# Optimization experiments

Hardware: AMD Instinct MI355X
Metric: run time of the kernel (lower is better)

The kernel has to match this reference:

```python
import jax, jax.numpy as jnp
import numpy as np

N = 50000          # nodes
E = 800000         # edges (avg degree 16)
IN_NODE = 64
IN_EDGE = 16
HID = 64
HEADS = 2
NEG_SLOPE = 0.2
EPS = 1e-16


def setup_inputs() -> dict:
    key = jax.random.key(0)
    ks = jax.random.split(key, 32)
    i = iter(range(32))
    rn = lambda shape, s=1.0: jax.random.normal(ks[next(i)], shape, jnp.float32) * s
    inp = {
        "h": rn((N, IN_NODE)),
        "e": rn((E, IN_EDGE)),
        "edge_index": jax.random.randint(ks[next(i)], (2, E), 0, N),
        "w": rn((E, IN_EDGE)),
        # initial GATConv: in_node -> hidden, heads=2 (averaged)
        "W0": rn((IN_NODE, HEADS * HID), 0.05),
        "att_src0": rn((HEADS, HID), 0.05),
        "att_dst0": rn((HEADS, HID), 0.05),
        "We0": rn((IN_EDGE, HEADS * HID), 0.05),
        "att_e0": rn((HEADS, HID), 0.05),
        "b0": jnp.zeros((HID,), jnp.float32),
        # hidden GATConv 1: hidden -> hidden, heads=1
        "W1": rn((HID, HID), 0.05),
        "att_src1": rn((1, HID), 0.05),
        "att_dst1": rn((1, HID), 0.05),
        "We1": rn((IN_EDGE, HID), 0.05),
        "att_e1": rn((1, HID), 0.05),
        "b1": jnp.zeros((HID,), jnp.float32),
        # hidden GATConv 2
        "W2": rn((HID, HID), 0.05),
        "att_src2": rn((1, HID), 0.05),
        "att_dst2": rn((1, HID), 0.05),
        "We2": rn((IN_EDGE, HID), 0.05),
        "att_e2": rn((1, HID), 0.05),
        "b2": jnp.zeros((HID,), jnp.float32),
        # readout Linear(hidden, in_node)
        "Wr": rn((HID, IN_NODE), 0.05),
        "br": jnp.zeros((IN_NODE,), jnp.float32),
    }
    return inp


def gat_conv(x, edge_attr, src, dst, W, a_src, a_dst, We, a_e, b, concat):
    """PyG-style GATConv with edge features (no self-loops)."""
    H, C = a_src.shape
    xw = (x @ W).reshape(-1, H, C)                      # [N, H, C]
    ew = (edge_attr @ We).reshape(-1, H, C)             # [E, H, C]
    alpha_n_src = jnp.einsum('nhc,hc->nh', xw, a_src)   # [N, H]
    alpha_n_dst = jnp.einsum('nhc,hc->nh', xw, a_dst)   # [N, H]
    alpha_e = jnp.einsum('ehc,hc->eh', ew, a_e)         # [E, H]
    alpha = alpha_n_src[src] + alpha_n_dst[dst] + alpha_e
    alpha = jax.nn.leaky_relu(alpha, NEG_SLOPE)         # [E, H]
    # segment softmax over incoming edges of each dst node
    m = jax.ops.segment_max(alpha, dst, num_segments=N)
    ex = jnp.exp(alpha - m[dst])
    den = jax.ops.segment_sum(ex, dst, num_segments=N)
    coef = ex / (den[dst] + EPS)                        # [E, H]
    msg = coef[:, :, None] * xw[src]                    # [E, H, C]
    out = jax.ops.segment_sum(msg, dst, num_segments=N) # [N, H, C]
    out = out.reshape(N, H * C) if concat else out.mean(axis=1)
    return out + b


def reference(h, e, edge_index, w,
              W0, att_src0, att_dst0, We0, att_e0, b0,
              W1, att_src1, att_dst1, We1, att_e1, b1,
              W2, att_src2, att_dst2, We2, att_e2, b2,
              Wr, br):
    src, dst = edge_index[0], edge_index[1]
    x = jax.nn.silu(gat_conv(h, w, src, dst, W0, att_src0, att_dst0, We0, att_e0, b0, concat=False))
    x = jax.nn.silu(gat_conv(x, w, src, dst, W1, att_src1, att_dst1, We1, att_e1, b1, concat=False))
    x = jax.nn.silu(gat_conv(x, w, src, dst, W2, att_src2, att_dst2, We2, att_e2, b2, concat=False))
    x = x @ Wr + br                                     # readout [N, IN_NODE]
    return (x, e)
```

## Files before the change

### kernel.cpp

```cpp
#include <hip/hip_runtime.h>
#include <hip/hip_bf16.h>

#define IN_NODE 64
#define IN_EDGE 16
#define HID 64
#define BKT_SHIFT 8
#define PART_T 1563
#define PART_TMAX 1600

using f32x4 = __attribute__((ext_vector_type(4))) float;
using f32x2 = __attribute__((ext_vector_type(2))) float;
using bf16x8 = __attribute__((ext_vector_type(8))) short;
#define MFMA16(a, b, c) __builtin_amdgcn_mfma_f32_16x16x32_bf16(a, b, c, 0, 0, 0)

__device__ __forceinline__ unsigned short f32_to_bf16u(float f) {
    __hip_bfloat16 hb = __float2bfloat16(f);
    return *(unsigned short*)&hb;
}
__device__ __forceinline__ float bf16u_to_f32(unsigned short u) {
    return __uint_as_float(((unsigned)u) << 16);
}


__global__ void copy4_kernel(const float4* __restrict__ in, float4* __restrict__ out, int n4) {
    int i = blockIdx.x * blockDim.x + threadIdx.x;
    if (i < n4) out[i] = in[i];
}

__global__ void prep_q_kernel(const float* __restrict__ We0, const float* __restrict__ ae0,
                              const float* __restrict__ We1, const float* __restrict__ ae1,
                              const float* __restrict__ We2, const float* __restrict__ ae2,
                              float* __restrict__ q) {
    int t = threadIdx.x;
    if (t < 32) {
        int k = t >> 1, h = t & 1;
        float s = 0.f;
        for (int c = 0; c < HID; ++c) s += We0[k * 128 + h * 64 + c] * ae0[h * 64 + c];
        q[k * 4 + h] = s;
    } else if (t < 48) {
        int k = t - 32;
        float s = 0.f;
        for (int c = 0; c < HID; ++c) s += We1[k * 64 + c] * ae1[c];
        q[k * 4 + 2] = s;
    } else {
        int k = t - 48;
        float s = 0.f;
        for (int c = 0; c < HID; ++c) s += We2[k * 64 + c] * ae2[c];
        q[k * 4 + 3] = s;
    }
}


__global__ void hist_kernel(const int* __restrict__ dst, int* __restrict__ counts, int E) {
    int e = blockIdx.x * blockDim.x + threadIdx.x;
    if (e < E) atomicAdd(&counts[dst[e]], 1);
}

__global__ __launch_bounds__(256) void scan_sums_kernel(const int* __restrict__ counts,
                                                        int* __restrict__ bsums, int n) {
    __shared__ int sd[256];
    int bbase = blockIdx.x * 1024;
    int s = 0;
    for (int i = threadIdx.x; i < 1024; i += 256) {
        int idx = bbase + i;
        s += (idx < n) ? counts[idx] : 0;
    }
    sd[threadIdx.x] = s;
    __syncthreads();
    for (int off = 128; off > 0; off >>= 1) {
        if (threadIdx.x < off) sd[threadIdx.x] += sd[threadIdx.x + off];
        __syncthreads();
    }
    if (threadIdx.x == 0) bsums[blockIdx.x] = sd[0];
}

__global__ __launch_bounds__(256) void scan_bsums_kernel(int* __restrict__ bsums, int nb) {
    __shared__ int sd[256];
    int t = threadIdx.x;
    int v = (t < nb) ? bsums[t] : 0;
    sd[t] = v;
    __syncthreads();
    for (int off = 1; off < 256; off <<= 1) {
        int tmp = (t >= off) ? sd[t - off] : 0;
        __syncthreads();
        sd[t] += tmp;
        __syncthreads();
    }
    if (t < nb) bsums[t] = sd[t] - v;
}

__global__ __launch_bounds__(256) void scan_write_kernel(const int* __restrict__ counts,
                                                         const int* __restrict__ bsums,
                                                         int* __restrict__ row_ptr, int n) {
    __shared__ int sd[256];
    int bbase = blockIdx.x * 1024;
    int t = threadIdx.x;
    int c[4];
    int ts = 0;
#pragma unroll
    for (int j = 0; j < 4; ++j) {
        int idx = bbase + t * 4 + j;
        c[j] = (idx < n) ? counts[idx] : 0;
        ts += c[j];
    }
    sd[t] = ts;
    __syncthreads();
    for (int off = 1; off < 256; off <<= 1) {
        int tmp = (t >= off) ? sd[t - off] : 0;
        __syncthreads();
        sd[t] += tmp;
        __syncthreads();
    }
    int texc = sd[t] - ts;
    int run = bsums[blockIdx.x] + texc;
#pragma unroll
    for (int j = 0; j < 4; ++j) {
        int idx = bbase + t * 4 + j;
        if (idx < n) {
            row_ptr[idx] = run;
            run += c[j];
            if (idx == n - 1) row_ptr[n] = run;
        }
    }
}


__global__ void init_gbcur_kernel(const int* __restrict__ row_ptr, int* __restrict__ gbcur,
                                  int NBK) {
    int t = blockIdx.x * blockDim.x + threadIdx.x;
    if (t < NBK) gbcur[t] = row_ptr[t << BKT_SHIFT];
}

__global__ __launch_bounds__(256) void partition_kernel(
    const int* __restrict__ dst, const int* __restrict__ src, const float* __restrict__ w,
    const float* __restrict__ q, int* __restrict__ gbcur, unsigned* __restrict__ part_sd,
    float4* __restrict__ part_ae4, int E, int NBK) {
    __shared__ int lhist[256];
    __shared__ int ldelta[256];
    __shared__ float qs[64];
    __shared__ unsigned s_sd[PART_TMAX];
    __shared__ float4 s_ae4[PART_TMAX];
    __shared__ unsigned char s_bkt[PART_TMAX];
    const int t = threadIdx.x;
    const int e0 = blockIdx.x * PART_T;
    const int e1 = min(e0 + PART_T, E);
    const int cnt_total = e1 - e0;
    if (t < 64) qs[t] = q[t];
    lhist[t] = 0;
    __syncthreads();
    for (int eb = e0 + t; eb < e1; eb += 1024) {
        int b4[4];
        bool v4[4];
#pragma unroll
        for (int j = 0; j < 4; ++j) {
            int e = eb + j * 256;
            v4[j] = e < e1;
            b4[j] = dst[v4[j] ? e : e0] >> BKT_SHIFT;
        }
#pragma unroll
        for (int j = 0; j < 4; ++j)
            if (v4[j]) atomicAdd(&lhist[b4[j]], 1);
    }
    __syncthreads();
    int cnt = lhist[t];
    __syncthreads();
    lhist[t] = cnt;
    __syncthreads();
    for (int off = 1; off < 256; off <<= 1) {
        int tmp = (t >= off) ? lhist[t - off] : 0;
        __syncthreads();
        lhist[t] += tmp;
        __syncthreads();
    }
    int lbase = lhist[t] - cnt;
    int gbase = (t < NBK && cnt) ? atomicAdd(&gbcur[t], cnt) : 0;
    ldelta[t] = gbase - lbase;
    __syncthreads();
    lhist[t] = lbase;
    __syncthreads();
    for (int eb = e0 + t; eb < e1; eb += 1024) {
        int d4[4], s4[4];
        bool v4[4];
        float4 a4[4];
#pragma unroll
        for (int j = 0; j < 4; ++j) {
            int e = eb + j * 256;
            v4[j] = e < e1;
            int ec = v4[j] ? e : e0;
            d4[j] = dst[ec];
            s4[j] = src[ec];
            const float4* w4p = (const float4*)(w + (size_t)ec * IN_EDGE);
            float a0 = 0.f, a1 = 0.f, a2 = 0.f, a3 = 0.f;
#pragma unroll
            for (int kq = 0; kq < 4; ++kq) {
                float4 wv = w4p[kq];
                float wk[4] = {wv.x, wv.y, wv.z, wv.w};
#pragma unroll
                for (int tt = 0; tt < 4; ++tt) {
                    int k = kq * 4 + tt;
                    a0 += wk[tt] * qs[k * 4 + 0];
                    a1 += wk[tt] * qs[k * 4 + 1];
                    a2 += wk[tt] * qs[k * 4 + 2];
                    a3 += wk[tt] * qs[k * 4 + 3];
                }
            }
            a4[j] = make_float4(a0, a1, a2, a3);
        }
#pragma unroll
        for (int j = 0; j < 4; ++j) {
            if (v4[j]) {
                int b = d4[j] >> BKT_SHIFT;
                int slot = atomicAdd(&lhist[b], 1);
                s_sd[slot] = ((unsigned)d4[j] << 16) | (unsigned)s4[j];
                s_ae4[slot] = a4[j];
                s_bkt[slot] = (unsigned char)b;
            }
        }
    }
    __syncthreads();
    for (int r = t; r < cnt_total; r += 256) {
        int b = s_bkt[r];
        int g = ldelta[b] + r;
        part_sd[g] = s_sd[r];
        part_ae4[g] = s_ae4[r];
    }
}

__global__ __launch_bounds__(256) void bucket_scatter_kernel(
    const unsigned* __restrict__ part_sd, const float4* __restrict__ part_ae4,
    const int* __restrict__ row_ptr, unsigned short* __restrict__ csr_src,
    float2* __restrict__ ae01, float* __restrict__ ae2, float* __restrict__ ae3, int N) {
    __shared__ int cur[256];
    const int t = threadIdx.x;
    const int node0 = blockIdx.x << BKT_SHIFT;
    const int nend = min(node0 + 256, N);
    if (t < nend - node0) cur[t] = row_ptr[node0 + t];
    __syncthreads();
    const int p0 = row_ptr[node0];
    const int p1 = row_ptr[nend];
    for (int pb = p0 + t; pb < p1; pb += 1024) {
        unsigned sd4[4];
        float4 a4[4];
        bool v4[4];
#pragma unroll
        for (int j = 0; j < 4; ++j) {
            int pp = pb + j * 256;
            v4[j] = pp < p1;
            int pc = v4[j] ? pp : p0;
            sd4[j] = part_sd[pc];
            a4[j] = part_ae4[pc];
        }
#pragma unroll
        for (int j = 0; j < 4; ++j) {
            if (v4[j]) {
                int d = (int)(sd4[j] >> 16);
                int slot = atomicAdd(&cur[d - node0], 1);
                csr_src[slot] = (unsigned short)(sd4[j] & 0xffffu);
                ae01[slot] = make_float2(a4[j].x, a4[j].y);
                ae2[slot] = a4[j].z;
                ae3[slot] = a4[j].w;
            }
        }
    }
}


__device__ __forceinline__ bf16x8 bfrag_w(const float* __restrict__ W, int ldc, int k0, int c) {
    bf16x8 f;
#pragma unroll
    for (int j = 0; j < 8; ++j) f[j] = (short)f32_to_bf16u(W[(k0 + j) * ldc + c]);
    return f;
}

__device__ __forceinline__ bf16x8 afrag_f32(const float* __restrict__ row, int k0) {
    float4 u = *(const float4*)(row + k0);
    float4 v = *(const float4*)(row + k0 + 4);
    bf16x8 f;
    f[0] = (short)f32_to_bf16u(u.x);
    f[1] = (short)f32_to_bf16u(u.y);
    f[2] = (short)f32_to_bf16u(u.z);
    f[3] = (short)f32_to_bf16u(u.w);
    f[4] = (short)f32_to_bf16u(v.x);
    f[5] = (short)f32_to_bf16u(v.y);
    f[6] = (short)f32_to_bf16u(v.z);
    f[7] = (short)f32_to_bf16u(v.w);
    return f;
}

template <int H, bool ABF16>
__global__ __launch_bounds__(256) void xw_alpha_mfma_kernel(
    const float* __restrict__ xf, const unsigned short* __restrict__ xb,
    const float* __restrict__ W, const float* __restrict__ a_src, const float* __restrict__ a_dst,
    unsigned char* __restrict__ xwb, float* __restrict__ alpha_src,
    float* __restrict__ alpha_dst, int ntiles) {
    const int lane = threadIdx.x & 63;
    const int wv = threadIdx.x >> 6;
    const int tile = blockIdx.x * 4 + wv;
    if (tile >= ntiles) return;
    const int cl = lane & 15, kg = lane >> 4;
    const int n0 = tile * 16;

    bf16x8 bf[2][4 * H];
    float asr[4 * H], adr[4 * H];
#pragma unroll
    for (int kt = 0; kt < 2; ++kt)
#pragma unroll
        for (int ct = 0; ct < 4 * H; ++ct)
            bf[kt][ct] = bfrag_w(W, 64 * H, kt * 32 + kg * 8, ct * 16 + cl);
#pragma unroll
    for (int ct = 0; ct < 4 * H; ++ct) {
        int hh = ct >> 2;
        int c = (ct & 3) * 16 + cl;
        asr[ct] = a_src[hh * 64 + c];
        adr[ct] = a_dst[hh * 64 + c];
    }

    bf16x8 af0, af1;
    if (ABF16) {
        const unsigned short* rp = xb + (size_t)(n0 + cl) * 64;
        af0 = *(const bf16x8*)(rp + kg * 8);
        af1 = *(const bf16x8*)(rp + 32 + kg * 8);
    } else {
        const float* rp = xf + (size_t)(n0 + cl) * 64;
        af0 = afrag_f32(rp, kg * 8);
        af1 = afrag_f32(rp, 32 + kg * 8);
    }

    f32x4 acc[4 * H];
#pragma unroll
    for (int ct = 0; ct < 4 * H; ++ct) {
        f32x4 z = {0.f, 0.f, 0.f, 0.f};
        z = MFMA16(af0, bf[0][ct], z);
        acc[ct] = MFMA16(af1, bf[1][ct], z);
    }

#pragma unroll
    for (int r = 0; r < 4; ++r) {
        int n = n0 + kg * 4 + r;
#pragma unroll
        for (int hh = 0; hh < H; ++hh) {
            int pk = 0;
            pk = __builtin_amdgcn_cvt_pk_fp8_f32(acc[hh * 4 + 0][r], acc[hh * 4 + 1][r], pk,
                                                 false);
            pk = __builtin_amdgcn_cvt_pk_fp8_f32(acc[hh * 4 + 2][r], acc[hh * 4 + 3][r], pk,
                                                 true);
            *(unsigned*)(xwb + ((size_t)n * H + hh) * 64 + cl * 4) = (unsigned)pk;
        }
    }

#pragma unroll
    for (int hh = 0; hh < H; ++hh) {
#pragma unroll
        for (int r = 0; r < 4; ++r) {
            float vs = 0.f, vd = 0.f;
#pragma unroll
            for (int q = 0; q < 4; ++q) {
                vs += acc[hh * 4 + q][r] * asr[hh * 4 + q];
                vd += acc[hh * 4 + q][r] * adr[hh * 4 + q];
            }
#pragma unroll
            for (int off = 8; off; off >>= 1) {
                vs += __shfl_xor(vs, off, 16);
                vd += __shfl_xor(vd, off, 16);
            }
            if (cl == r) {
                int n = n0 + kg * 4 + r;
                alpha_src[n * H + hh] = vs;
                alpha_dst[n * H + hh] = vd;
            }
        }
    }
}

__global__ __launch_bounds__(256) void readout_mfma_kernel(const unsigned short* __restrict__ xb,
                                                           const float* __restrict__ Wr,
                                                           const float* __restrict__ br,
                                                           float* __restrict__ out, int ntiles) {
    const int lane = threadIdx.x & 63;
    const int wv = threadIdx.x >> 6;
    const int tile = blockIdx.x * 4 + wv;
    if (tile >= ntiles) return;
    const int cl = lane & 15, kg = lane >> 4;
    const int n0 = tile * 16;

    bf16x8 bf[2][4];
    float brv[4];
#pragma unroll
    for (int kt = 0; kt < 2; ++kt)
#pragma unroll
        for (int ct = 0; ct < 4; ++ct) bf[kt][ct] = bfrag_w(Wr, 64, kt * 32 + kg * 8, ct * 16 + cl);
#pragma unroll
    for (int ct = 0; ct < 4; ++ct) brv[ct] = br[ct * 16 + cl];

    const unsigned short* rp = xb + (size_t)(n0 + cl) * 64;
    bf16x8 af0 = *(const bf16x8*)(rp + kg * 8);
    bf16x8 af1 = *(const bf16x8*)(rp + 32 + kg * 8);

    f32x4 acc[4];
#pragma unroll
    for (int ct = 0; ct < 4; ++ct) {
        f32x4 z = {0.f, 0.f, 0.f, 0.f};
        z = MFMA16(af0, bf[0][ct], z);
        acc[ct] = MFMA16(af1, bf[1][ct], z);
    }
#pragma unroll
    for (int r = 0; r < 4; ++r) {
        int n = n0 + kg * 4 + r;
#pragma unroll
        for (int ct = 0; ct < 4; ++ct) out[(size_t)n * 64 + ct * 16 + cl] = acc[ct][r] + brv[ct];
    }
}


template <int H, int AEOFF>
__global__ __launch_bounds__(256) void aggregate16_kernel(
    const unsigned char* __restrict__ xwb, const float* __restrict__ alpha_src,
    const float* __restrict__ alpha_dst, const void* __restrict__ aeplane,
    const int* __restrict__ row_ptr, const unsigned short* __restrict__ csr_src,
    const float* __restrict__ bias, unsigned short* __restrict__ x_out, int N) {
    const int l = threadIdx.x & 15;
    const int grp = threadIdx.x >> 4;
    const int n = blockIdx.x * 16 + grp;
    if (n >= N) return;
    const int base = row_ptr[n];
    const int deg = row_ptr[n + 1] - base;

    float bb[4];
#pragma unroll
    for (int q = 0; q < 4; ++q) bb[q] = bias[q * 16 + l];

    float m[H], den[H], o[H][4], ad[H];
#pragma unroll
    for (int h = 0; h < H; ++h) {
        m[h] = -1e30f;
        den[h] = 0.f;
        o[h][0] = o[h][1] = o[h][2] = o[h][3] = 0.f;
        ad[h] = alpha_dst[n * H + h];
    }

    for (int start = 0; start < deg; start += 16) {
        int j = start + l;
        bool act = j < deg;
        int s = 0;
        float a[H], ev[H];
        if (act) {
            s = csr_src[base + j];
            float asv[H], aev[H];
            if (H == 2) {
                float2 ae = ((const float2*)aeplane)[base + j];
                aev[0] = ae.x;
                aev[H - 1] = ae.y;
                float2 as2 = *((const float2*)alpha_src + s);
                asv[0] = as2.x;
                asv[H - 1] = as2.y;
            } else {
                aev[0] = ((const float*)aeplane)[base + j];
                asv[0] = alpha_src[s];
            }
#pragma unroll
            for (int h = 0; h < H; ++h) {
                float av = asv[h] + ad[h] + aev[h];
                a[h] = (av > 0.f) ? av : 0.2f * av;
            }
        } else {
#pragma unroll
            for (int h = 0; h < H; ++h) a[h] = -1e30f;
        }
        int cnt = min(deg - start, 16);
#pragma unroll
        for (int h = 0; h < H; ++h) {
            float cm = a[h];
#pragma unroll
            for (int off = 8; off; off >>= 1) cm = fmaxf(cm, __shfl_xor(cm, off, 16));
            float m_new = fmaxf(m[h], cm);
            float scale = __expf(m[h] - m_new);
            ev[h] = act ? __expf(a[h] - m_new) : 0.f;
            float cs = ev[h];
#pragma unroll
            for (int off = 8; off; off >>= 1) cs += __shfl_xor(cs, off, 16);
            den[h] = den[h] * scale + cs;
#pragma unroll
            for (int q = 0; q < 4; ++q) o[h][q] *= scale;
            m[h] = m_new;
        }
#pragma unroll 8
        for (int jj = 0; jj < cnt; ++jj) {
            int sj = __shfl(s, jj, 16);
#pragma unroll
            for (int h = 0; h < H; ++h) {
                float ej = __shfl(ev[h], jj, 16);
                unsigned v = *((const unsigned*)(xwb + ((size_t)sj * H + h) * 64) + l);
                f32x2 lo = __builtin_amdgcn_cvt_pk_f32_fp8((int)v, false);
                f32x2 hi = __builtin_amdgcn_cvt_pk_f32_fp8((int)v, true);
                o[h][0] += ej * lo[0];
                o[h][1] += ej * lo[1];
                o[h][2] += ej * hi[0];
                o[h][3] += ej * hi[1];
            }
        }
    }

#pragma unroll
    for (int q = 0; q < 4; ++q) {
        float acc = 0.f;
#pragma unroll
        for (int h = 0; h < H; ++h) acc += o[h][q] / (den[h] + 1e-16f);
        float r = acc * (H == 2 ? 0.5f : 1.f) + bb[q];
        r = r / (1.f + __expf(-r));
        x_out[(size_t)n * 64 + q * 16 + l] = f32_to_bf16u(r);
    }
}


static inline char* carve(char*& p, size_t bytes) {
    char* r = p;
    p += (bytes + 255) & ~(size_t)255;
    return r;
}

extern "C" void kernel_launch(void* const* d_in, const int* in_sizes, int n_in, void* d_out,
                              int out_size, void* d_ws, size_t ws_size, hipStream_t stream) {
    const int N = in_sizes[0] / IN_NODE;
    const int E = in_sizes[1] / IN_EDGE;

    const float* h = (const float*)d_in[0];
    const float* e = (const float*)d_in[1];
    const int* edge_index = (const int*)d_in[2];
    const float* w = (const float*)d_in[3];
    const float* W0 = (const float*)d_in[4];
    const float* as0 = (const float*)d_in[5];
    const float* ad0 = (const float*)d_in[6];
    const float* We0 = (const float*)d_in[7];
    const float* ae0 = (const float*)d_in[8];
    const float* b0 = (const float*)d_in[9];
    const float* W1 = (const float*)d_in[10];
    const float* as1 = (const float*)d_in[11];
    const float* ad1 = (const float*)d_in[12];
    const float* We1 = (const float*)d_in[13];
    const float* ae1 = (const float*)d_in[14];
    const float* b1 = (const float*)d_in[15];
    const float* W2 = (const float*)d_in[16];
    const float* as2 = (const float*)d_in[17];
    const float* ad2 = (const float*)d_in[18];
    const float* We2 = (const float*)d_in[19];
    const float* ae2 = (const float*)d_in[20];
    const float* b2 = (const float*)d_in[21];
    const float* Wr = (const float*)d_in[22];
    const float* br = (const float*)d_in[23];

    const int* src = edge_index;
    const int* dst = edge_index + E;

    float* out_x = (float*)d_out;
    float* out_e = (float*)d_out + (size_t)N * IN_NODE;

    char* p = (char*)d_ws;
    unsigned char* xwb = (unsigned char*)carve(p, (size_t)N * 128);
    unsigned short* xA = (unsigned short*)carve(p, (size_t)N * 64 * 2);
    unsigned short* xB = (unsigned short*)carve(p, (size_t)N * 64 * 2);
    float* csr_ae01 = (float*)carve(p, (size_t)E * 2 * 4);
    float* csr_ae2 = (float*)carve(p, (size_t)E * 4);
    float* csr_ae3 = (float*)carve(p, (size_t)E * 4);
    float* a_src = (float*)carve(p, (size_t)N * 2 * 4);
    float* a_dst = (float*)carve(p, (size_t)N * 2 * 4);
    float* qall = (float*)carve(p, 64 * 4);
    int* row_ptr = (int*)carve(p, (size_t)(N + 1) * 4);
    int* counts = (int*)carve(p, (size_t)N * 4);
    int* bsums = (int*)carve(p, 256 * 4);
    unsigned short* csr_src = (unsigned short*)carve(p, (size_t)E * 2);
    unsigned* part_sd = (unsigned*)carve(p, (size_t)E * 4);
    float* part_ae4 = (float*)carve(p, (size_t)E * 4 * 4);
    int* gbcur = (int*)carve(p, 1024 * 4);

    const int egrid = (E + 255) / 256;
    const int ngrid16 = (N + 15) / 16;
    const int NB = (N + 1023) / 1024;
    const int NBK = (N + 255) >> BKT_SHIFT;
    const int PART_BLOCKS = (E + PART_T - 1) / PART_T;
    const int ntiles = (N + 15) / 16;
    const int ggrid = (ntiles + 3) / 4;

    hipMemsetAsync(counts, 0, (size_t)N * 4, stream);
    hist_kernel<<<egrid, 256, 0, stream>>>(dst, counts, E);
    scan_sums_kernel<<<NB, 256, 0, stream>>>(counts, bsums, N);
    scan_bsums_kernel<<<1, 256, 0, stream>>>(bsums, NB);
    scan_write_kernel<<<NB, 256, 0, stream>>>(counts, bsums, row_ptr, N);

    prep_q_kernel<<<1, 64, 0, stream>>>(We0, ae0, We1, ae1, We2, ae2, qall);

    init_gbcur_kernel<<<(NBK + 255) / 256, 256, 0, stream>>>(row_ptr, gbcur, NBK);
    partition_kernel<<<PART_BLOCKS, 256, 0, stream>>>(dst, src, w, qall, gbcur, part_sd,
                                                      (float4*)part_ae4, E, NBK);
    bucket_scatter_kernel<<<NBK, 256, 0, stream>>>(part_sd, (const float4*)part_ae4, row_ptr,
                                                   csr_src, (float2*)csr_ae01, csr_ae2, csr_ae3,
                                                   N);

    {
        int n4 = E * IN_EDGE / 4;
        copy4_kernel<<<(n4 + 255) / 256, 256, 0, stream>>>((const float4*)e, (float4*)out_e, n4);
    }

    xw_alpha_mfma_kernel<2, false><<<ggrid, 256, 0, stream>>>(h, nullptr, W0, as0, ad0, xwb, a_src,
                                                              a_dst, ntiles);
    aggregate16_kernel<2, 0><<<ngrid16, 256, 0, stream>>>(xwb, a_src, a_dst, csr_ae01, row_ptr,
                                                          csr_src, b0, xA, N);
    xw_alpha_mfma_kernel<1, true><<<ggrid, 256, 0, stream>>>(nullptr, xA, W1, as1, ad1, xwb, a_src,
                                                             a_dst, ntiles);
    aggregate16_kernel<1, 2><<<ngrid16, 256, 0, stream>>>(xwb, a_src, a_dst, csr_ae2, row_ptr,
                                                          csr_src, b1, xB, N);
    xw_alpha_mfma_kernel<1, true><<<ggrid, 256, 0, stream>>>(nullptr, xB, W2, as2, ad2, xwb, a_src,
                                                             a_dst, ntiles);
    aggregate16_kernel<1, 3><<<ngrid16, 256, 0, stream>>>(xwb, a_src, a_dst, csr_ae3, row_ptr,
                                                          csr_src, b2, xA, N);
    readout_mfma_kernel<<<ggrid, 256, 0, stream>>>(xA, Wr, br, out_x, ntiles);
}
```

Baseline: 231.6 us.

## Replace per-node histogram and global scan with per-bucket counts and local scans

The per-node histogram with global atomics and the three-kernel prefix scan over N counts is replaced by a bucket-level histogram (256-node buckets, shared-memory atomics) and a single-block scan over the bucket totals. Per-node row pointers are now computed inside bucket_scatter_kernel, which counts its own bucket's edges in shared memory and scans them before scattering. This drops several kernel launches, the N-sized memset, and global atomic contention. In exchange the scatter kernel makes an extra pass over part_sd.

```diff
diff --git a/kernel.cpp b/kernel.cpp
--- a/kernel.cpp
+++ b/kernel.cpp
@@ -51,33 +51,26 @@
 }
 
 
-__global__ void hist_kernel(const int* __restrict__ dst, int* __restrict__ counts, int E) {
-    int e = blockIdx.x * blockDim.x + threadIdx.x;
-    if (e < E) atomicAdd(&counts[dst[e]], 1);
-}
-
-__global__ __launch_bounds__(256) void scan_sums_kernel(const int* __restrict__ counts,
-                                                        int* __restrict__ bsums, int n) {
-    __shared__ int sd[256];
-    int bbase = blockIdx.x * 1024;
-    int s = 0;
-    for (int i = threadIdx.x; i < 1024; i += 256) {
-        int idx = bbase + i;
-        s += (idx < n) ? counts[idx] : 0;
-    }
-    sd[threadIdx.x] = s;
-    __syncthreads();
-    for (int off = 128; off > 0; off >>= 1) {
-        if (threadIdx.x < off) sd[threadIdx.x] += sd[threadIdx.x + off];
-        __syncthreads();
-    }
-    if (threadIdx.x == 0) bsums[blockIdx.x] = sd[0];
-}
-
-__global__ __launch_bounds__(256) void scan_bsums_kernel(int* __restrict__ bsums, int nb) {
+__global__ __launch_bounds__(256) void btot_kernel(const int* __restrict__ dst,
+                                                   int* __restrict__ btot, int E, int NBK) {
+    __shared__ int lhist[256];
+    const int t = threadIdx.x;
+    lhist[t] = 0;
+    __syncthreads();
+    const int stride = gridDim.x * 256;
+    for (int e = blockIdx.x * 256 + t; e < E; e += stride) atomicAdd(&lhist[dst[e] >> BKT_SHIFT], 1);
+    __syncthreads();
+    if (t < NBK && lhist[t]) atomicAdd(&btot[t], lhist[t]);
+}
+
+__global__ __launch_bounds__(256) void scan_btot_kernel(const int* __restrict__ btot,
+                                                        int* __restrict__ bbase,
+                                                        int* __restrict__ gbcur,
+                                                        int* __restrict__ row_ptr, int NBK, int N,
+                                                        int E) {
     __shared__ int sd[256];
     int t = threadIdx.x;
-    int v = (t < nb) ? bsums[t] : 0;
+    int v = (t < NBK) ? btot[t] : 0;
     sd[t] = v;
     __syncthreads();
     for (int off = 1; off < 256; off <<= 1) {
@@ -86,50 +79,15 @@
         sd[t] += tmp;
         __syncthreads();
     }
-    if (t < nb) bsums[t] = sd[t] - v;
-}
-
-__global__ __launch_bounds__(256) void scan_write_kernel(const int* __restrict__ counts,
-                                                         const int* __restrict__ bsums,
-                                                         int* __restrict__ row_ptr, int n) {
-    __shared__ int sd[256];
-    int bbase = blockIdx.x * 1024;
-    int t = threadIdx.x;
-    int c[4];
-    int ts = 0;
-#pragma unroll
-    for (int j = 0; j < 4; ++j) {
-        int idx = bbase + t * 4 + j;
-        c[j] = (idx < n) ? counts[idx] : 0;
-        ts += c[j];
-    }
-    sd[t] = ts;
-    __syncthreads();
-    for (int off = 1; off < 256; off <<= 1) {
-        int tmp = (t >= off) ? sd[t - off] : 0;
-        __syncthreads();
-        sd[t] += tmp;
-        __syncthreads();
-    }
-    int texc = sd[t] - ts;
-    int run = bsums[blockIdx.x] + texc;
-#pragma unroll
-    for (int j = 0; j < 4; ++j) {
-        int idx = bbase + t * 4 + j;
-        if (idx < n) {
-            row_ptr[idx] = run;
-            run += c[j];
-            if (idx == n - 1) row_ptr[n] = run;
-        }
-    }
-}
-
-
-__global__ void init_gbcur_kernel(const int* __restrict__ row_ptr, int* __restrict__ gbcur,
-                                  int NBK) {
-    int t = blockIdx.x * blockDim.x + threadIdx.x;
-    if (t < NBK) gbcur[t] = row_ptr[t << BKT_SHIFT];
-}
+    int excl = sd[t] - v;
+    if (t < NBK) {
+        bbase[t] = excl;
+        gbcur[t] = excl;
+    }
+    if (t == NBK - 1) bbase[NBK] = sd[t];
+    if (t == 0) row_ptr[N] = E;
+}
+
 
 __global__ __launch_bounds__(256) void partition_kernel(
     const int* __restrict__ dst, const int* __restrict__ src, const float* __restrict__ w,
@@ -226,18 +184,48 @@
     }
 }
 
+
 __global__ __launch_bounds__(256) void bucket_scatter_kernel(
     const unsigned* __restrict__ part_sd, const float4* __restrict__ part_ae4,
-    const int* __restrict__ row_ptr, unsigned short* __restrict__ csr_src,
+    const int* __restrict__ bbase, int* __restrict__ row_ptr, unsigned short* __restrict__ csr_src,
     float2* __restrict__ ae01, float* __restrict__ ae2, float* __restrict__ ae3, int N) {
-    __shared__ int cur[256];
+    __shared__ int cnt[256];
     const int t = threadIdx.x;
     const int node0 = blockIdx.x << BKT_SHIFT;
     const int nend = min(node0 + 256, N);
-    if (t < nend - node0) cur[t] = row_ptr[node0 + t];
-    __syncthreads();
-    const int p0 = row_ptr[node0];
-    const int p1 = row_ptr[nend];
+    const int p0 = bbase[blockIdx.x];
+    const int p1 = bbase[blockIdx.x + 1];
+    cnt[t] = 0;
+    __syncthreads();
+    for (int pb = p0 + t; pb < p1; pb += 1024) {
+        int d4[4];
+        bool v4[4];
+#pragma unroll
+        for (int j = 0; j < 4; ++j) {
+            int pp = pb + j * 256;
+            v4[j] = pp < p1;
+            d4[j] = (int)(part_sd[v4[j] ? pp : p0] >> 16);
+        }
+#pragma unroll
+        for (int j = 0; j < 4; ++j)
+            if (v4[j]) atomicAdd(&cnt[d4[j] - node0], 1);
+    }
+    __syncthreads();
+    int c = cnt[t];
+    __syncthreads();
+    cnt[t] = c;
+    __syncthreads();
+    for (int off = 1; off < 256; off <<= 1) {
+        int tmp = (t >= off) ? cnt[t - off] : 0;
+        __syncthreads();
+        cnt[t] += tmp;
+        __syncthreads();
+    }
+    int excl = cnt[t] - c;
+    if (node0 + t < nend) row_ptr[node0 + t] = p0 + excl;
+    __syncthreads();
+    cnt[t] = p0 + excl;
+    __syncthreads();
     for (int pb = p0 + t; pb < p1; pb += 1024) {
         unsigned sd4[4];
         float4 a4[4];
@@ -254,7 +242,7 @@
         for (int j = 0; j < 4; ++j) {
             if (v4[j]) {
                 int d = (int)(sd4[j] >> 16);
-                int slot = atomicAdd(&cur[d - node0], 1);
+                int slot = atomicAdd(&cnt[d - node0], 1);
                 csr_src[slot] = (unsigned short)(sd4[j] & 0xffffu);
                 ae01[slot] = make_float2(a4[j].x, a4[j].y);
                 ae2[slot] = a4[j].z;
@@ -565,35 +553,30 @@
     float* a_dst = (float*)carve(p, (size_t)N * 2 * 4);
     float* qall = (float*)carve(p, 64 * 4);
     int* row_ptr = (int*)carve(p, (size_t)(N + 1) * 4);
-    int* counts = (int*)carve(p, (size_t)N * 4);
-    int* bsums = (int*)carve(p, 256 * 4);
+    int* btot = (int*)carve(p, 256 * 4);
+    int* bbase = (int*)carve(p, 257 * 4);
     unsigned short* csr_src = (unsigned short*)carve(p, (size_t)E * 2);
     unsigned* part_sd = (unsigned*)carve(p, (size_t)E * 4);
     float* part_ae4 = (float*)carve(p, (size_t)E * 4 * 4);
     int* gbcur = (int*)carve(p, 1024 * 4);
 
-    const int egrid = (E + 255) / 256;
     const int ngrid16 = (N + 15) / 16;
-    const int NB = (N + 1023) / 1024;
     const int NBK = (N + 255) >> BKT_SHIFT;
     const int PART_BLOCKS = (E + PART_T - 1) / PART_T;
     const int ntiles = (N + 15) / 16;
     const int ggrid = (ntiles + 3) / 4;
 
-    hipMemsetAsync(counts, 0, (size_t)N * 4, stream);
-    hist_kernel<<<egrid, 256, 0, stream>>>(dst, counts, E);
-    scan_sums_kernel<<<NB, 256, 0, stream>>>(counts, bsums, N);
-    scan_bsums_kernel<<<1, 256, 0, stream>>>(bsums, NB);
-    scan_write_kernel<<<NB, 256, 0, stream>>>(counts, bsums, row_ptr, N);
+    hipMemsetAsync(btot, 0, 256 * 4, stream);
+    btot_kernel<<<512, 256, 0, stream>>>(dst, btot, E, NBK);
+    scan_btot_kernel<<<1, 256, 0, stream>>>(btot, bbase, gbcur, row_ptr, NBK, N, E);
 
     prep_q_kernel<<<1, 64, 0, stream>>>(We0, ae0, We1, ae1, We2, ae2, qall);
 
-    init_gbcur_kernel<<<(NBK + 255) / 256, 256, 0, stream>>>(row_ptr, gbcur, NBK);
     partition_kernel<<<PART_BLOCKS, 256, 0, stream>>>(dst, src, w, qall, gbcur, part_sd,
                                                       (float4*)part_ae4, E, NBK);
-    bucket_scatter_kernel<<<NBK, 256, 0, stream>>>(part_sd, (const float4*)part_ae4, row_ptr,
-                                                   csr_src, (float2*)csr_ae01, csr_ae2, csr_ae3,
-                                                   N);
+    bucket_scatter_kernel<<<NBK, 256, 0, stream>>>(part_sd, (const float4*)part_ae4, bbase,
+                                                   row_ptr, csr_src, (float2*)csr_ae01, csr_ae2,
+                                                   csr_ae3, N);
 
     {
         int n4 = E * IN_EDGE / 4;
```

Result: faster. 205.8 us (-11.2%).
